# Kernel optimization log

Hardware: AMD Instinct MI355X
Metric: run time of the kernel (lower is better)

## Reference

```python
import jax, jax.numpy as jnp
import numpy as np

CODEBOOK_SIZE = 1024
D_MODEL = 512
NUM_SAMPLES = 10
TEMP = 1.0
COMMITMENT_COST = 0.25
PADDING_IDX = 0


def setup_inputs() -> dict:
    key = jax.random.key(0)
    k1, k2, k3 = jax.random.split(key, 3)
    inputs = jax.random.normal(k1, (64, 512, D_MODEL), dtype=jnp.float32)
    padding_mask = jax.random.randint(k2, (64, 512), 0, 2) == 1
    codebook_weight = 0.02 * jax.random.normal(k3, (CODEBOOK_SIZE, D_MODEL), dtype=jnp.float32)
    codebook_weight = codebook_weight.at[PADDING_IDX].set(0.0)  # padding_idx row zeroed
    return {"inputs": inputs, "padding_mask": padding_mask, "codebook_weight": codebook_weight}


def reference(inputs, padding_mask, codebook_weight):
    B, S, D = inputs.shape
    K = codebook_weight.shape[0]
    flat = inputs.reshape(-1, D)  # [N, D]
    # squared-euclidean distances to codebook entries: [N, K]
    dist = (jnp.sum(flat * flat, axis=1, keepdims=True)
            + jnp.sum(codebook_weight * codebook_weight, axis=1)
            - 2.0 * (flat @ codebook_weight.T))
    pad = padding_mask.reshape(-1)  # [N]
    col = jnp.arange(K)
    # padded rows: only code 0 allowed; non-padded rows: code 0 disallowed
    allowed = jnp.where(pad[:, None], col == 0, col != 0)
    dist = jnp.where(allowed, dist, jnp.inf)

    # Multinomial(total_count=NUM_SAMPLES, logits=-dist/TEMP): draw NUM_SAMPLES
    # categorical samples per row and count them.
    logits = -dist / TEMP
    N = flat.shape[0]
    draws = jax.random.categorical(jax.random.key(42), logits, axis=-1,
                                   shape=(NUM_SAMPLES, N))  # [num_samples, N]
    row_idx = jnp.broadcast_to(jnp.arange(N)[None, :], draws.shape)
    samples = jnp.zeros((N, K), jnp.float32).at[row_idx, draws].add(1.0)  # counts, [N, K]

    quantized = (samples @ codebook_weight).reshape(B, S, D) / NUM_SAMPLES

    num_nonpad = (jnp.sum(~pad) * D).astype(jnp.float32)
    e_latent_loss = jnp.sum((jax.lax.stop_gradient(quantized) - inputs) ** 2) / num_nonpad
    loss = COMMITMENT_COST * e_latent_loss

    # straight-through estimator
    quantized_st = inputs + jax.lax.stop_gradient(quantized - inputs)

    avg_probs = jnp.mean(samples, axis=0) / NUM_SAMPLES  # [K]
    perplexity = jnp.exp(-jnp.sum(avg_probs * jnp.log(avg_probs + 1e-10)))

    samples_out = samples.reshape(B, S, K)
    return quantized_st, samples_out, loss, perplexity
```

## Files before the change

kernel.cpp:

```cpp
#include <hip/hip_runtime.h>
#include <stdint.h>

#define NROWS 32768
#define KC 1024
#define DM 512
#define NKPROD 33554432u

typedef _Float16 v8h __attribute__((ext_vector_type(8)));
typedef float v4f __attribute__((ext_vector_type(4)));

__device__ __forceinline__ uint32_t rotl32(uint32_t x, int d) {
  return __builtin_amdgcn_alignbit(x, x, 32 - d);
}

__device__ __forceinline__ void threefry_x2(uint32_t xa, uint32_t xb,
                                            uint32_t& oa, uint32_t& ob) {
  const uint32_t ks1 = 42u, ks2 = 0x1BD11BF0u;
  uint32_t a0 = 0u, a1 = xa + ks1;
  uint32_t b0 = 0u, b1 = xb + ks1;
#define R2(r) { a0 += a1; b0 += b1; a1 = rotl32(a1, r); b1 = rotl32(b1, r); a1 ^= a0; b1 ^= b0; }
  R2(13) R2(15) R2(26) R2(6)
  a0 += ks1; b0 += ks1; a1 += ks2 + 1u; b1 += ks2 + 1u;
  R2(17) R2(29) R2(16) R2(24)
  a0 += ks2; b0 += ks2; a1 += 2u; b1 += 2u;
  R2(13) R2(15) R2(26) R2(6)
  a1 += ks1 + 3u; b1 += ks1 + 3u;
  R2(17) R2(29) R2(16) R2(24)
  a0 += ks1; b0 += ks1; a1 += ks2 + 4u; b1 += ks2 + 4u;
  R2(13) R2(15) R2(26) R2(6)
  a0 += ks2; b0 += ks2; a1 += 5u; b1 += 5u;
#undef R2
  oa = a0 ^ a1;
  ob = b0 ^ b1;
}

__global__ __launch_bounds__(256) void k_count(const uint8_t* __restrict__ mb,
                                               uint32_t* __restrict__ flag,
                                               int* __restrict__ cntB,
                                               int* __restrict__ cntI) {
  __shared__ int sB[256], sI[256];
  int t = threadIdx.x, b = blockIdx.x;
  int T = b * 256 + t;
  uint32_t f = 0;
#pragma unroll
  for (int i = 0; i < 2; ++i) {
    int bi = T * 2 + i;
    if ((bi & 3) && mb[bi]) f = 1;
  }
  if (f) atomicOr(flag, 1u);
  const int* mi = (const int*)mb;
  int r0 = b * 512 + t * 2;
  int cB = 0, cI = 0;
#pragma unroll
  for (int i = 0; i < 2; ++i) {
    int r = r0 + i;
    cB += (mb[r] == 0) ? 1 : 0;
    cI += (mi[r] == 0) ? 1 : 0;
  }
  sB[t] = cB; sI[t] = cI;
  __syncthreads();
  for (int off = 128; off; off >>= 1) {
    if (t < off) { sB[t] += sB[t + off]; sI[t] += sI[t + off]; }
    __syncthreads();
  }
  if (t == 0) { cntB[b] = sB[0]; cntI[b] = sI[0]; }
}

__global__ __launch_bounds__(256) void k_scatter(const uint8_t* __restrict__ mb,
                                                 const uint32_t* __restrict__ flag,
                                                 const int* __restrict__ cntB,
                                                 const int* __restrict__ cntI,
                                                 int* __restrict__ idx,
                                                 int* __restrict__ npp) {
  __shared__ int sc[256];
  int t = threadIdx.x, b = blockIdx.x;
  bool isbool = (*flag) != 0;
  const int* mi = (const int*)mb;
  const int* cnt = isbool ? cntB : cntI;
  int pre = 0, tot = 0;
  for (int j = 0; j < 64; ++j) {
    int c = cnt[j];
    if (j < b) pre += c;
    tot += c;
  }
  int r0 = b * 512 + t * 2;
  bool np0 = isbool ? (mb[r0] == 0)     : (mi[r0] == 0);
  bool np1 = isbool ? (mb[r0 + 1] == 0) : (mi[r0 + 1] == 0);
  int my = (int)np0 + (int)np1;
  sc[t] = my;
  __syncthreads();
  for (int off = 1; off < 256; off <<= 1) {
    int v = (t >= off) ? sc[t - off] : 0;
    __syncthreads();
    sc[t] += v;
    __syncthreads();
  }
  int excl = sc[t] - my;
  int npPos = pre + excl;
  int padPos = tot + (b * 512 - pre) + (t * 2 - excl);
  if (np0) idx[npPos++] = r0;     else idx[padPos++] = r0;
  if (np1) idx[npPos]   = r0 + 1; else idx[padPos]   = r0 + 1;
  if (b == 0 && t == 0) *npp = tot;
}

__global__ __launch_bounds__(256) void k_asplit(const float* __restrict__ A,
                                                const int* __restrict__ idx,
                                                _Float16* __restrict__ Ah2,
                                                _Float16* __restrict__ Al2,
                                                float* __restrict__ An) {
  int slot = blockIdx.x * 4 + (threadIdx.x >> 6);
  int l = threadIdx.x & 63;
  int n = idx[slot];
  const float* ap = A + (size_t)n * DM + l * 8;
  float x[8];
  *(float4*)&x[0] = *(const float4*)ap;
  *(float4*)&x[4] = *(const float4*)(ap + 4);
  _Float16 h[8], lo[8];
  float s = 0.f;
#pragma unroll
  for (int i = 0; i < 8; ++i) {
    _Float16 hh = (_Float16)x[i];
    h[i] = hh; lo[i] = (_Float16)(x[i] - (float)hh);
    s = fmaf(x[i], x[i], s);
  }
  *(v8h*)&Ah2[(size_t)slot * DM + l * 8] = *(v8h*)h;
  *(v8h*)&Al2[(size_t)slot * DM + l * 8] = *(v8h*)lo;
#pragma unroll
  for (int off = 32; off; off >>= 1) s += __shfl_xor(s, off, 64);
  if (l == 0) An[slot] = s;
}

__global__ __launch_bounds__(256) void k_bsplit(const float* __restrict__ B,
                                                _Float16* __restrict__ Bh2,
                                                _Float16* __restrict__ Bl2,
                                                float* __restrict__ Bn) {
  int k = blockIdx.x * 4 + (threadIdx.x >> 6);
  int l = threadIdx.x & 63;
  const float* bp = B + (size_t)k * DM + l * 8;
  float x[8];
  *(float4*)&x[0] = *(const float4*)bp;
  *(float4*)&x[4] = *(const float4*)(bp + 4);
  _Float16 h[8], lo[8];
  float s = 0.f;
#pragma unroll
  for (int i = 0; i < 8; ++i) {
    _Float16 hh = (_Float16)x[i];
    h[i] = hh; lo[i] = (_Float16)(x[i] - (float)hh);
    s = fmaf(x[i], x[i], s);
  }
  *(v8h*)&Bh2[(size_t)k * DM + l * 8] = *(v8h*)h;
  *(v8h*)&Bl2[(size_t)k * DM + l * 8] = *(v8h*)lo;
#pragma unroll
  for (int off = 32; off; off >>= 1) s += __shfl_xor(s, off, 64);
  if (l == 0) Bn[k] = s;
}

#define LDK 40
__global__ __launch_bounds__(256) void k_gemm5(const _Float16* __restrict__ Ah2,
                                               const _Float16* __restrict__ Al2,
                                               const float* __restrict__ An,
                                               const _Float16* __restrict__ Bh2,
                                               const _Float16* __restrict__ Bl2,
                                               const float* __restrict__ Bn,
                                               const int* __restrict__ idx,
                                               const int* __restrict__ npp,
                                               float* __restrict__ S) {
  int NP = *npp;
  int bx = blockIdx.x & 7;
  int by = blockIdx.x >> 3;
  int r0 = by * 128, c0 = bx * 128;
  if (r0 >= NP) return;

  __shared__ _Float16 Ah[128 * LDK], Al[128 * LDK];
  __shared__ _Float16 Bh[128 * LDK], Bl[128 * LDK];

  int tid = threadIdx.x;
  int wid = tid >> 6;
  int wr = wid >> 1, wc = wid & 1;
  int l = tid & 63;
  int lr = l & 15;
  int k8 = (l >> 4) * 8;

  int srow = tid >> 1;
  int ssub = (tid & 1) * 16;

  const _Float16* ahg = Ah2 + (size_t)(r0 + srow) * DM + ssub;
  const _Float16* alg = Al2 + (size_t)(r0 + srow) * DM + ssub;
  const _Float16* bhg = Bh2 + (size_t)(c0 + srow) * DM + ssub;
  const _Float16* blg = Bl2 + (size_t)(c0 + srow) * DM + ssub;

  v4f acc[4][4];
#pragma unroll
  for (int m = 0; m < 4; ++m)
#pragma unroll
    for (int n = 0; n < 4; ++n) acc[m][n] = (v4f)0.0f;

  for (int k0 = 0; k0 < DM; k0 += 32) {
    v8h ah0 = *(const v8h*)(ahg + k0);
    v8h ah1 = *(const v8h*)(ahg + k0 + 8);
    v8h al0 = *(const v8h*)(alg + k0);
    v8h al1 = *(const v8h*)(alg + k0 + 8);
    v8h bh0 = *(const v8h*)(bhg + k0);
    v8h bh1 = *(const v8h*)(bhg + k0 + 8);
    v8h bl0 = *(const v8h*)(blg + k0);
    v8h bl1 = *(const v8h*)(blg + k0 + 8);
    __syncthreads();
    int wb = srow * LDK + ssub;
    *(v8h*)&Ah[wb]     = ah0;
    *(v8h*)&Ah[wb + 8] = ah1;
    *(v8h*)&Al[wb]     = al0;
    *(v8h*)&Al[wb + 8] = al1;
    *(v8h*)&Bh[wb]     = bh0;
    *(v8h*)&Bh[wb + 8] = bh1;
    *(v8h*)&Bl[wb]     = bl0;
    *(v8h*)&Bl[wb + 8] = bl1;
    __syncthreads();

    v8h fah[4], fal[4];
#pragma unroll
    for (int m = 0; m < 4; ++m) {
      int row = wr * 64 + m * 16 + lr;
      fah[m] = *(const v8h*)&Ah[row * LDK + k8];
      fal[m] = *(const v8h*)&Al[row * LDK + k8];
    }
#pragma unroll
    for (int n = 0; n < 4; ++n) {
      int col = wc * 64 + n * 16 + lr;
      v8h fbh = *(const v8h*)&Bh[col * LDK + k8];
      v8h fbl = *(const v8h*)&Bl[col * LDK + k8];
#pragma unroll
      for (int m = 0; m < 4; ++m) {
        acc[m][n] = __builtin_amdgcn_mfma_f32_16x16x32_f16(fah[m], fbh, acc[m][n], 0, 0, 0);
        acc[m][n] = __builtin_amdgcn_mfma_f32_16x16x32_f16(fah[m], fbl, acc[m][n], 0, 0, 0);
        acc[m][n] = __builtin_amdgcn_mfma_f32_16x16x32_f16(fal[m], fbh, acc[m][n], 0, 0, 0);
      }
    }
  }

  float cnp[4];
#pragma unroll
  for (int n = 0; n < 4; ++n) cnp[n] = Bn[c0 + wc * 64 + n * 16 + lr];

#pragma unroll
  for (int m = 0; m < 4; ++m) {
    int rl = wr * 64 + m * 16 + (l >> 4) * 4;
#pragma unroll
    for (int r = 0; r < 4; ++r) {
      int org = idx[r0 + rl + r];
      float rq = An[r0 + rl + r];
      float* sp = S + (size_t)org * KC + c0;
#pragma unroll
      for (int n = 0; n < 4; ++n) {
        int cl = wc * 64 + n * 16 + lr;
        sp[cl] = -((rq + cnp[n]) - 2.0f * acc[m][n][r]);
      }
    }
  }
}

__global__ __launch_bounds__(256) void k_pad(const float* __restrict__ X,
                                             const int* __restrict__ idx,
                                             const int* __restrict__ npp,
                                             float* __restrict__ qout,
                                             float* __restrict__ sout,
                                             double* __restrict__ esum) {
  int NP = *npp;
  int slot = blockIdx.x * 4 + (threadIdx.x >> 6);
  if (slot < NP) return;
  int n = idx[slot];
  int l = threadIdx.x & 63;

  float* so = sout + (size_t)n * KC + l * 16;
  float4 z = make_float4(0.f, 0.f, 0.f, 0.f);
  *(float4*)(so)      = (l == 0) ? make_float4(10.f, 0.f, 0.f, 0.f) : z;
  *(float4*)(so + 4)  = z;
  *(float4*)(so + 8)  = z;
  *(float4*)(so + 12) = z;

  const float* xr = X + (size_t)n * DM + l * 8;
  float4 x0 = *(const float4*)xr, x1 = *(const float4*)(xr + 4);
  float* qo = qout + (size_t)n * DM + l * 8;
  *(float4*)qo       = z;
  *(float4*)(qo + 4) = z;
  double ls = (double)(x0.x*x0.x) + (double)(x0.y*x0.y)
            + (double)(x0.z*x0.z) + (double)(x0.w*x0.w)
            + (double)(x1.x*x1.x) + (double)(x1.y*x1.y)
            + (double)(x1.z*x1.z) + (double)(x1.w*x1.w);
#pragma unroll
  for (int off = 32; off; off >>= 1) ls += __shfl_xor(ls, off, 64);
  if (l == 0) atomicAdd(&esum[n & 63], ls);
}

__global__ __launch_bounds__(256, 8) void k_sample_i(
    const float* __restrict__ S, const float* __restrict__ X,
    const float* __restrict__ CW, const int* __restrict__ idx,
    const int* __restrict__ npp,
    float* __restrict__ qout, float* __restrict__ sout,
    float* __restrict__ cnt, double* __restrict__ esum) {
  int NP = *npp;
  int slot = blockIdx.x * 4 + (threadIdx.x >> 6);
  if (slot >= NP) return;
  int n = idx[slot];
  int l = threadIdx.x & 63;
  int base = l * 16;
  const float* srow = S + (size_t)n * KC + base;

  float lmax;
  {
    float lg0[16];
#pragma unroll
    for (int j = 0; j < 16; j += 4)
      *(float4*)&lg0[j] = *(const float4*)(srow + j);
    if (l == 0) lg0[0] = -__builtin_inff();
    lmax = lg0[0];
#pragma unroll
    for (int i = 1; i < 16; ++i) lmax = fmaxf(lmax, lg0[i]);
#pragma unroll
    for (int off = 32; off; off >>= 1)
      lmax = fmaxf(lmax, __shfl_xor(lmax, off, 64));
  }

  float bv[10];
  uint32_t bi[10];
#pragma unroll
  for (int s = 0; s < 10; ++s) { bv[s] = -__builtin_inff(); bi[s] = 0xFFFFFFFFu; }

  uint32_t tb0 = (uint32_t)n * (uint32_t)KC + (uint32_t)base;
#pragma unroll 1
  for (int j = 0; j < 16; ++j) {
    float lgj = srow[j];
    uint32_t kk = (uint32_t)(base + j);
    if (kk == 0u) lgj = -__builtin_inff();
    float mj = 0.69314718056f * __expf(lmax - lgj);
    uint32_t t0 = tb0 + (uint32_t)j;
#pragma unroll
    for (int sp = 0; sp < 5; ++sp) {
      uint32_t ba, bb;
      threefry_x2(t0 + (uint32_t)(2 * sp) * NKPROD,
                  t0 + (uint32_t)(2 * sp + 1) * NKPROD, ba, bb);
      float fa = __uint_as_float((ba >> 9) | 0x3F800000u) - 1.0f;
      float fb = __uint_as_float((bb >> 9) | 0x3F800000u) - 1.0f;
      float ua = fmaxf(1.17549435e-38f, fa);
      float ub = fmaxf(1.17549435e-38f, fb);
      float va = __log2f(ua) * mj;
      float vb = __log2f(ub) * mj;
      if (va > bv[2 * sp])     { bv[2 * sp] = va;     bi[2 * sp] = kk; }
      if (vb > bv[2 * sp + 1]) { bv[2 * sp + 1] = vb; bi[2 * sp + 1] = kk; }
    }
  }

#pragma unroll
  for (int s = 0; s < 10; ++s) {
#pragma unroll
    for (int off = 32; off; off >>= 1) {
      float ov = __shfl_xor(bv[s], off, 64);
      uint32_t oi = __shfl_xor(bi[s], off, 64);
      if (ov > bv[s] || (ov == bv[s] && oi < bi[s])) { bv[s] = ov; bi[s] = oi; }
    }
  }

  float* so = sout + (size_t)n * KC + base;
#pragma unroll
  for (int j4 = 0; j4 < 16; j4 += 4) {
    float c[4];
#pragma unroll
    for (int i = 0; i < 4; ++i) {
      uint32_t k = (uint32_t)(base + j4 + i);
      float cc = 0.f;
#pragma unroll
      for (int s = 0; s < 10; ++s) cc += (bi[s] == k) ? 1.f : 0.f;
      c[i] = cc;
    }
    *(float4*)(so + j4) = make_float4(c[0], c[1], c[2], c[3]);
  }

  float q[8];
#pragma unroll
  for (int i = 0; i < 8; ++i) q[i] = 0.f;
#pragma unroll
  for (int s = 0; s < 10; ++s) {
    const float* cr = CW + (size_t)bi[s] * DM + l * 8;
    float4 g0 = *(const float4*)cr;
    float4 g1 = *(const float4*)(cr + 4);
    q[0] += g0.x; q[1] += g0.y; q[2] += g0.z; q[3] += g0.w;
    q[4] += g1.x; q[5] += g1.y; q[6] += g1.z; q[7] += g1.w;
    if (l == 0) atomicAdd(&cnt[bi[s]], 1.0f);
  }

  const float* xr = X + (size_t)n * DM + l * 8;
  float4 x0 = *(const float4*)xr, x1 = *(const float4*)(xr + 4);
  float xs[8] = {x0.x, x0.y, x0.z, x0.w, x1.x, x1.y, x1.z, x1.w};
  float st[8];
  double ls = 0.0;
#pragma unroll
  for (int j = 0; j < 8; ++j) {
    float qq = q[j] / 10.0f;
    float d = qq - xs[j];
    ls += (double)(d * d);
    st[j] = xs[j] + d;
  }
  float* qo = qout + (size_t)n * DM + l * 8;
  *(float4*)qo       = make_float4(st[0], st[1], st[2], st[3]);
  *(float4*)(qo + 4) = make_float4(st[4], st[5], st[6], st[7]);

#pragma unroll
  for (int off = 32; off; off >>= 1) ls += __shfl_xor(ls, off, 64);
  if (l == 0) atomicAdd(&esum[n & 63], ls);
}

__global__ __launch_bounds__(256) void k_final(const int* __restrict__ npp,
                                               const float* __restrict__ cnt,
                                               const double* __restrict__ esum,
                                               float* __restrict__ scal) {
  __shared__ double snd[256];
  int t = threadIdx.x;
  int npad = NROWS - *npp;
  double ss = 0.0;
  for (int k = t; k < KC; k += 256) {
    float c = (k == 0) ? (float)(npad * 10) : cnt[k];
    float p = c / 327680.0f;
    ss += (double)(p * logf(p + 1e-10f));
  }
  snd[t] = ss;
  __syncthreads();
  for (int off = 128; off; off >>= 1) {
    if (t < off) snd[t] += snd[t + off];
    __syncthreads();
  }
  if (t == 0) {
    double es = 0.0;
    for (int i = 0; i < 64; ++i) es += esum[i];
    float num_nonpad = (float)((NROWS - npad) * DM);
    float el = (float)es / num_nonpad;
    scal[0] = 0.25f * el;
    scal[1] = expf(-(float)snd[0]);
  }
}

extern "C" void kernel_launch(void* const* d_in, const int* in_sizes, int n_in,
                              void* d_out, int out_size, void* d_ws, size_t ws_size,
                              hipStream_t stream) {
  const float* X  = (const float*)d_in[0];
  const void*  M  = d_in[1];
  const float* CW = (const float*)d_in[2];
  float* out  = (float*)d_out;
  float* qout = out;
  float* sout = out + 16777216;
  float* scal = out + 50331648;
  _Float16* Ah2 = (_Float16*)qout;
  _Float16* Al2 = Ah2 + 16777216;
  uint8_t* ws = (uint8_t*)d_ws;
  double*   esum = (double*)ws;
  uint32_t* flag = (uint32_t*)(ws + 512);
  int*      npp  = (int*)(ws + 768);
  float*    cnt  = (float*)(ws + 1024);
  int*      cntB = (int*)(ws + 5120);
  int*      cntI = (int*)(ws + 5376);
  int*      idx  = (int*)(ws + 8192);
  float*    An   = (float*)(ws + 139264);
  _Float16* Bh2  = (_Float16*)(ws + 270336);
  _Float16* Bl2  = (_Float16*)(ws + 270336 + 1048576);
  float*    Bn   = (float*)(ws + 270336 + 2097152);
  (void)in_sizes; (void)n_in; (void)out_size; (void)ws_size;

  hipMemsetAsync(d_ws, 0, 8192, stream);
  k_count<<<64, 256, 0, stream>>>((const uint8_t*)M, flag, cntB, cntI);
  k_scatter<<<64, 256, 0, stream>>>((const uint8_t*)M, flag, cntB, cntI, idx, npp);
  k_asplit<<<8192, 256, 0, stream>>>(X, idx, Ah2, Al2, An);
  k_bsplit<<<256, 256, 0, stream>>>(CW, Bh2, Bl2, Bn);
  k_gemm5<<<2048, 256, 0, stream>>>(Ah2, Al2, An, Bh2, Bl2, Bn, idx, npp, sout);
  k_pad<<<8192, 256, 0, stream>>>(X, idx, npp, qout, sout, esum);
  k_sample_i<<<8192, 256, 0, stream>>>(sout, X, CW, idx, npp, qout, sout, cnt, esum);
  k_final<<<1, 256, 0, stream>>>(npp, cnt, esum, scal);
}
```

Baseline: 508.7 us.

## Fuse A-split, GEMM, padding and sampling into one persistent work-queue kernel

Replaces the separate asplit, gemm, pad and sample kernels with one persistent kernel. Helper blocks pull GEMM tiles from an atomic ticket counter and split the fp32 inputs into fp16 hi/lo parts on the fly, so the split arrays never go through HBM. The remaining blocks handle padded rows, and then all blocks pull sampling work and spin on per-row-group completion counters. The codebook split is folded into the count kernel. This removes launches and the intermediate A traffic, but adds spin-waits, atomics and a dependence on enough blocks being co-resident to avoid stalls.

Result: slower. 988.5 us (+94.3%).

```diff
diff --git a/kernel.cpp b/kernel.cpp
--- a/kernel.cpp
+++ b/kernel.cpp
@@ -5,6 +5,8 @@
 #define KC 1024
 #define DM 512
 #define NKPROD 33554432u
+#define NHELP 256
+#define LDK 40
 
 typedef _Float16 v8h __attribute__((ext_vector_type(8)));
 typedef float v4f __attribute__((ext_vector_type(4)));
@@ -34,10 +36,32 @@
   ob = b0 ^ b1;
 }
 
-__global__ __launch_bounds__(256) void k_count(const uint8_t* __restrict__ mb,
-                                               uint32_t* __restrict__ flag,
-                                               int* __restrict__ cntB,
-                                               int* __restrict__ cntI) {
+__global__ __launch_bounds__(256) void k_count_bsplit(
+    const uint8_t* __restrict__ mb, const float* __restrict__ B,
+    uint32_t* __restrict__ flag, int* __restrict__ cntB, int* __restrict__ cntI,
+    _Float16* __restrict__ Bh2, _Float16* __restrict__ Bl2, float* __restrict__ Bn) {
+  if (blockIdx.x >= 64) {
+    int k = (blockIdx.x - 64) * 4 + (threadIdx.x >> 6);
+    int l = threadIdx.x & 63;
+    const float* bp = B + (size_t)k * DM + l * 8;
+    float x[8];
+    *(float4*)&x[0] = *(const float4*)bp;
+    *(float4*)&x[4] = *(const float4*)(bp + 4);
+    _Float16 h[8], lo[8];
+    float s = 0.f;
+#pragma unroll
+    for (int i = 0; i < 8; ++i) {
+      _Float16 hh = (_Float16)x[i];
+      h[i] = hh; lo[i] = (_Float16)(x[i] - (float)hh);
+      s = fmaf(x[i], x[i], s);
+    }
+    *(v8h*)&Bh2[(size_t)k * DM + l * 8] = *(v8h*)h;
+    *(v8h*)&Bl2[(size_t)k * DM + l * 8] = *(v8h*)lo;
+#pragma unroll
+    for (int off = 32; off; off >>= 1) s += __shfl_xor(s, off, 64);
+    if (l == 0) Bn[k] = s;
+    return;
+  }
   __shared__ int sB[256], sI[256];
   int t = threadIdx.x, b = blockIdx.x;
   int T = b * 256 + t;
@@ -103,309 +127,289 @@
   if (b == 0 && t == 0) *npp = tot;
 }
 
-__global__ __launch_bounds__(256) void k_asplit(const float* __restrict__ A,
-                                                const int* __restrict__ idx,
-                                                _Float16* __restrict__ Ah2,
-                                                _Float16* __restrict__ Al2,
-                                                float* __restrict__ An) {
-  int slot = blockIdx.x * 4 + (threadIdx.x >> 6);
-  int l = threadIdx.x & 63;
-  int n = idx[slot];
-  const float* ap = A + (size_t)n * DM + l * 8;
-  float x[8];
-  *(float4*)&x[0] = *(const float4*)ap;
-  *(float4*)&x[4] = *(const float4*)(ap + 4);
-  _Float16 h[8], lo[8];
-  float s = 0.f;
-#pragma unroll
-  for (int i = 0; i < 8; ++i) {
-    _Float16 hh = (_Float16)x[i];
-    h[i] = hh; lo[i] = (_Float16)(x[i] - (float)hh);
-    s = fmaf(x[i], x[i], s);
-  }
-  *(v8h*)&Ah2[(size_t)slot * DM + l * 8] = *(v8h*)h;
-  *(v8h*)&Al2[(size_t)slot * DM + l * 8] = *(v8h*)lo;
-#pragma unroll
-  for (int off = 32; off; off >>= 1) s += __shfl_xor(s, off, 64);
-  if (l == 0) An[slot] = s;
-}
-
-__global__ __launch_bounds__(256) void k_bsplit(const float* __restrict__ B,
-                                                _Float16* __restrict__ Bh2,
-                                                _Float16* __restrict__ Bl2,
-                                                float* __restrict__ Bn) {
-  int k = blockIdx.x * 4 + (threadIdx.x >> 6);
-  int l = threadIdx.x & 63;
-  const float* bp = B + (size_t)k * DM + l * 8;
-  float x[8];
-  *(float4*)&x[0] = *(const float4*)bp;
-  *(float4*)&x[4] = *(const float4*)(bp + 4);
-  _Float16 h[8], lo[8];
-  float s = 0.f;
-#pragma unroll
-  for (int i = 0; i < 8; ++i) {
-    _Float16 hh = (_Float16)x[i];
-    h[i] = hh; lo[i] = (_Float16)(x[i] - (float)hh);
-    s = fmaf(x[i], x[i], s);
-  }
-  *(v8h*)&Bh2[(size_t)k * DM + l * 8] = *(v8h*)h;
-  *(v8h*)&Bl2[(size_t)k * DM + l * 8] = *(v8h*)lo;
-#pragma unroll
-  for (int off = 32; off; off >>= 1) s += __shfl_xor(s, off, 64);
-  if (l == 0) Bn[k] = s;
-}
-
-#define LDK 40
-__global__ __launch_bounds__(256) void k_gemm5(const _Float16* __restrict__ Ah2,
-                                               const _Float16* __restrict__ Al2,
-                                               const float* __restrict__ An,
-                                               const _Float16* __restrict__ Bh2,
-                                               const _Float16* __restrict__ Bl2,
-                                               const float* __restrict__ Bn,
-                                               const int* __restrict__ idx,
-                                               const int* __restrict__ npp,
-                                               float* __restrict__ S) {
+__global__ __launch_bounds__(256, 4) void k_mega(
+    const float* __restrict__ X, const float* __restrict__ CW,
+    const _Float16* __restrict__ Bh2, const _Float16* __restrict__ Bl2,
+    const float* __restrict__ Bn,
+    const int* __restrict__ idx, const int* __restrict__ npp,
+    float* __restrict__ S, float* __restrict__ qout,
+    float* __restrict__ cnt, double* __restrict__ esum,
+    int* __restrict__ gc, int* __restrict__ pc, int* __restrict__ scc,
+    int* __restrict__ gemmDone) {
+  __shared__ _Float16 AhS[128 * LDK], AlS[128 * LDK];
+  __shared__ _Float16 BhS[128 * LDK], BlS[128 * LDK];
+  __shared__ int sticket;
   int NP = *npp;
-  int bx = blockIdx.x & 7;
-  int by = blockIdx.x >> 3;
-  int r0 = by * 128, c0 = bx * 128;
-  if (r0 >= NP) return;
-
-  __shared__ _Float16 Ah[128 * LDK], Al[128 * LDK];
-  __shared__ _Float16 Bh[128 * LDK], Bl[128 * LDK];
-
+  int ngroups = (NP + 127) >> 7;
+  int NTG = ngroups << 3;
+  int NPAD = NROWS - NP;
+  int NTP = (NPAD + 15) >> 4;
+  int NTS = (NP + 3) >> 2;
   int tid = threadIdx.x;
-  int wid = tid >> 6;
-  int wr = wid >> 1, wc = wid & 1;
-  int l = tid & 63;
-  int lr = l & 15;
-  int k8 = (l >> 4) * 8;
-
-  int srow = tid >> 1;
-  int ssub = (tid & 1) * 16;
-
-  const _Float16* ahg = Ah2 + (size_t)(r0 + srow) * DM + ssub;
-  const _Float16* alg = Al2 + (size_t)(r0 + srow) * DM + ssub;
-  const _Float16* bhg = Bh2 + (size_t)(c0 + srow) * DM + ssub;
-  const _Float16* blg = Bl2 + (size_t)(c0 + srow) * DM + ssub;
-
-  v4f acc[4][4];
-#pragma unroll
-  for (int m = 0; m < 4; ++m)
-#pragma unroll
-    for (int n = 0; n < 4; ++n) acc[m][n] = (v4f)0.0f;
-
-  for (int k0 = 0; k0 < DM; k0 += 32) {
-    v8h ah0 = *(const v8h*)(ahg + k0);
-    v8h ah1 = *(const v8h*)(ahg + k0 + 8);
-    v8h al0 = *(const v8h*)(alg + k0);
-    v8h al1 = *(const v8h*)(alg + k0 + 8);
-    v8h bh0 = *(const v8h*)(bhg + k0);
-    v8h bh1 = *(const v8h*)(bhg + k0 + 8);
-    v8h bl0 = *(const v8h*)(blg + k0);
-    v8h bl1 = *(const v8h*)(blg + k0 + 8);
-    __syncthreads();
-    int wb = srow * LDK + ssub;
-    *(v8h*)&Ah[wb]     = ah0;
-    *(v8h*)&Ah[wb + 8] = ah1;
-    *(v8h*)&Al[wb]     = al0;
-    *(v8h*)&Al[wb + 8] = al1;
-    *(v8h*)&Bh[wb]     = bh0;
-    *(v8h*)&Bh[wb + 8] = bh1;
-    *(v8h*)&Bl[wb]     = bl0;
-    *(v8h*)&Bl[wb + 8] = bl1;
-    __syncthreads();
-
-    v8h fah[4], fal[4];
-#pragma unroll
-    for (int m = 0; m < 4; ++m) {
-      int row = wr * 64 + m * 16 + lr;
-      fah[m] = *(const v8h*)&Ah[row * LDK + k8];
-      fal[m] = *(const v8h*)&Al[row * LDK + k8];
+  int wid = tid >> 6, l = tid & 63;
+
+  if (blockIdx.x < NHELP) {
+    int wr = wid >> 1, wc = wid & 1;
+    int lr = l & 15, k8 = (l >> 4) * 8;
+    int srow = tid >> 1, ssub = (tid & 1) * 16;
+    while (true) {
+      __syncthreads();
+      if (tid == 0) sticket = atomicAdd(gc, 1);
+      __syncthreads();
+      int g = sticket;
+      if (g >= NTG) break;
+      int by = g >> 3, bx = g & 7;
+      int r0 = by << 7, c0 = bx << 7;
+      int orig = idx[r0 + srow];
+      const float* ag = X + (size_t)orig * DM + ssub;
+      const _Float16* bhg = Bh2 + (size_t)(c0 + srow) * DM + ssub;
+      const _Float16* blg = Bl2 + (size_t)(c0 + srow) * DM + ssub;
+
+      v4f acc[4][4];
+#pragma unroll
+      for (int m = 0; m < 4; ++m)
+#pragma unroll
+        for (int n = 0; n < 4; ++n) acc[m][n] = (v4f)0.0f;
+      float sqa = 0.f;
+
+      for (int k0 = 0; k0 < DM; k0 += 32) {
+        float xa[16];
+#pragma unroll
+        for (int i = 0; i < 16; i += 4)
+          *(float4*)&xa[i] = *(const float4*)(ag + k0 + i);
+        v8h bh0 = *(const v8h*)(bhg + k0);
+        v8h bh1 = *(const v8h*)(bhg + k0 + 8);
+        v8h bl0 = *(const v8h*)(blg + k0);
+        v8h bl1 = *(const v8h*)(blg + k0 + 8);
+        _Float16 ha[16], la[16];
+#pragma unroll
+        for (int i = 0; i < 16; ++i) {
+          float x = xa[i];
+          _Float16 h = (_Float16)x;
+          ha[i] = h; la[i] = (_Float16)(x - (float)h);
+          sqa = fmaf(x, x, sqa);
+        }
+        __syncthreads();
+        int wb = srow * LDK + ssub;
+        *(v8h*)&AhS[wb]     = *(v8h*)&ha[0];
+        *(v8h*)&AhS[wb + 8] = *(v8h*)&ha[8];
+        *(v8h*)&AlS[wb]     = *(v8h*)&la[0];
+        *(v8h*)&AlS[wb + 8] = *(v8h*)&la[8];
+        *(v8h*)&BhS[wb]     = bh0;
+        *(v8h*)&BhS[wb + 8] = bh1;
+        *(v8h*)&BlS[wb]     = bl0;
+        *(v8h*)&BlS[wb + 8] = bl1;
+        __syncthreads();
+
+        v8h fah[4], fal[4];
+#pragma unroll
+        for (int m = 0; m < 4; ++m) {
+          int row = wr * 64 + m * 16 + lr;
+          fah[m] = *(const v8h*)&AhS[row * LDK + k8];
+          fal[m] = *(const v8h*)&AlS[row * LDK + k8];
+        }
+#pragma unroll
+        for (int n = 0; n < 4; ++n) {
+          int col = wc * 64 + n * 16 + lr;
+          v8h fbh = *(const v8h*)&BhS[col * LDK + k8];
+          v8h fbl = *(const v8h*)&BlS[col * LDK + k8];
+#pragma unroll
+          for (int m = 0; m < 4; ++m) {
+            acc[m][n] = __builtin_amdgcn_mfma_f32_16x16x32_f16(fah[m], fbh, acc[m][n], 0, 0, 0);
+            acc[m][n] = __builtin_amdgcn_mfma_f32_16x16x32_f16(fah[m], fbl, acc[m][n], 0, 0, 0);
+            acc[m][n] = __builtin_amdgcn_mfma_f32_16x16x32_f16(fal[m], fbh, acc[m][n], 0, 0, 0);
+          }
+        }
+      }
+
+      __syncthreads();
+      float* tmpf = (float*)AhS;
+      float* rsf  = (float*)AlS;
+      tmpf[tid] = sqa;
+      __syncthreads();
+      if ((tid & 1) == 0) rsf[srow] = tmpf[tid] + tmpf[tid + 1];
+      __syncthreads();
+
+      float cnp[4];
+#pragma unroll
+      for (int n = 0; n < 4; ++n) cnp[n] = Bn[c0 + wc * 64 + n * 16 + lr];
+
+#pragma unroll
+      for (int m = 0; m < 4; ++m) {
+        int rl = wr * 64 + m * 16 + (l >> 4) * 4;
+#pragma unroll
+        for (int r = 0; r < 4; ++r) {
+          int sl = r0 + rl + r;
+          if (sl < NP) {
+            int org = idx[sl];
+            float rq = rsf[rl + r];
+            float* sp = S + (size_t)org * KC + c0;
+#pragma unroll
+            for (int n = 0; n < 4; ++n) {
+              int cl = wc * 64 + n * 16 + lr;
+              sp[cl] = -((rq + cnp[n]) - 2.0f * acc[m][n][r]);
+            }
+          }
+        }
+      }
+      __threadfence();
+      __syncthreads();
+      if (tid == 0) atomicAdd(&gemmDone[by], 1);
     }
-#pragma unroll
-    for (int n = 0; n < 4; ++n) {
-      int col = wc * 64 + n * 16 + lr;
-      v8h fbh = *(const v8h*)&Bh[col * LDK + k8];
-      v8h fbl = *(const v8h*)&Bl[col * LDK + k8];
-#pragma unroll
-      for (int m = 0; m < 4; ++m) {
-        acc[m][n] = __builtin_amdgcn_mfma_f32_16x16x32_f16(fah[m], fbh, acc[m][n], 0, 0, 0);
-        acc[m][n] = __builtin_amdgcn_mfma_f32_16x16x32_f16(fah[m], fbl, acc[m][n], 0, 0, 0);
-        acc[m][n] = __builtin_amdgcn_mfma_f32_16x16x32_f16(fal[m], fbh, acc[m][n], 0, 0, 0);
+  } else {
+    while (true) {
+      __syncthreads();
+      if (tid == 0) sticket = atomicAdd(pc, 1);
+      __syncthreads();
+      int p = sticket;
+      if (p >= NTP) break;
+      for (int i = 0; i < 4; ++i) {
+        int ps = (p << 4) + (wid << 2) + i;
+        if (ps >= NPAD) break;
+        int n = idx[NP + ps];
+        float* so = S + (size_t)n * KC + l * 16;
+        float4 z = make_float4(0.f, 0.f, 0.f, 0.f);
+        *(float4*)(so)      = (l == 0) ? make_float4(10.f, 0.f, 0.f, 0.f) : z;
+        *(float4*)(so + 4)  = z;
+        *(float4*)(so + 8)  = z;
+        *(float4*)(so + 12) = z;
+        const float* xr = X + (size_t)n * DM + l * 8;
+        float4 x0 = *(const float4*)xr, x1 = *(const float4*)(xr + 4);
+        float* qo = qout + (size_t)n * DM + l * 8;
+        *(float4*)qo       = z;
+        *(float4*)(qo + 4) = z;
+        double ls = (double)(x0.x*x0.x) + (double)(x0.y*x0.y)
+                  + (double)(x0.z*x0.z) + (double)(x0.w*x0.w)
+                  + (double)(x1.x*x1.x) + (double)(x1.y*x1.y)
+                  + (double)(x1.z*x1.z) + (double)(x1.w*x1.w);
+#pragma unroll
+        for (int off = 32; off; off >>= 1) ls += __shfl_xor(ls, off, 64);
+        if (l == 0) atomicAdd(&esum[n & 63], ls);
       }
     }
   }
 
-  float cnp[4];
-#pragma unroll
-  for (int n = 0; n < 4; ++n) cnp[n] = Bn[c0 + wc * 64 + n * 16 + lr];
-
-#pragma unroll
-  for (int m = 0; m < 4; ++m) {
-    int rl = wr * 64 + m * 16 + (l >> 4) * 4;
-#pragma unroll
-    for (int r = 0; r < 4; ++r) {
-      int org = idx[r0 + rl + r];
-      float rq = An[r0 + rl + r];
-      float* sp = S + (size_t)org * KC + c0;
-#pragma unroll
-      for (int n = 0; n < 4; ++n) {
-        int cl = wc * 64 + n * 16 + lr;
-        sp[cl] = -((rq + cnp[n]) - 2.0f * acc[m][n][r]);
-      }
+  while (true) {
+    __syncthreads();
+    if (tid == 0) sticket = atomicAdd(scc, 1);
+    __syncthreads();
+    int st = sticket;
+    if (st >= NTS) break;
+    int g = (st << 2) >> 7;
+    if (tid == 0) {
+      while (atomicAdd(&gemmDone[g], 0) < 8) __builtin_amdgcn_s_sleep(32);
     }
-  }
-}
-
-__global__ __launch_bounds__(256) void k_pad(const float* __restrict__ X,
-                                             const int* __restrict__ idx,
-                                             const int* __restrict__ npp,
-                                             float* __restrict__ qout,
-                                             float* __restrict__ sout,
-                                             double* __restrict__ esum) {
-  int NP = *npp;
-  int slot = blockIdx.x * 4 + (threadIdx.x >> 6);
-  if (slot < NP) return;
-  int n = idx[slot];
-  int l = threadIdx.x & 63;
-
-  float* so = sout + (size_t)n * KC + l * 16;
-  float4 z = make_float4(0.f, 0.f, 0.f, 0.f);
-  *(float4*)(so)      = (l == 0) ? make_float4(10.f, 0.f, 0.f, 0.f) : z;
-  *(float4*)(so + 4)  = z;
-  *(float4*)(so + 8)  = z;
-  *(float4*)(so + 12) = z;
-
-  const float* xr = X + (size_t)n * DM + l * 8;
-  float4 x0 = *(const float4*)xr, x1 = *(const float4*)(xr + 4);
-  float* qo = qout + (size_t)n * DM + l * 8;
-  *(float4*)qo       = z;
-  *(float4*)(qo + 4) = z;
-  double ls = (double)(x0.x*x0.x) + (double)(x0.y*x0.y)
-            + (double)(x0.z*x0.z) + (double)(x0.w*x0.w)
-            + (double)(x1.x*x1.x) + (double)(x1.y*x1.y)
-            + (double)(x1.z*x1.z) + (double)(x1.w*x1.w);
-#pragma unroll
-  for (int off = 32; off; off >>= 1) ls += __shfl_xor(ls, off, 64);
-  if (l == 0) atomicAdd(&esum[n & 63], ls);
-}
-
-__global__ __launch_bounds__(256, 8) void k_sample_i(
-    const float* __restrict__ S, const float* __restrict__ X,
-    const float* __restrict__ CW, const int* __restrict__ idx,
-    const int* __restrict__ npp,
-    float* __restrict__ qout, float* __restrict__ sout,
-    float* __restrict__ cnt, double* __restrict__ esum) {
-  int NP = *npp;
-  int slot = blockIdx.x * 4 + (threadIdx.x >> 6);
-  if (slot >= NP) return;
-  int n = idx[slot];
-  int l = threadIdx.x & 63;
-  int base = l * 16;
-  const float* srow = S + (size_t)n * KC + base;
-
-  float lmax;
-  {
-    float lg0[16];
-#pragma unroll
-    for (int j = 0; j < 16; j += 4)
-      *(float4*)&lg0[j] = *(const float4*)(srow + j);
-    if (l == 0) lg0[0] = -__builtin_inff();
-    lmax = lg0[0];
-#pragma unroll
-    for (int i = 1; i < 16; ++i) lmax = fmaxf(lmax, lg0[i]);
-#pragma unroll
-    for (int off = 32; off; off >>= 1)
-      lmax = fmaxf(lmax, __shfl_xor(lmax, off, 64));
-  }
-
-  float bv[10];
-  uint32_t bi[10];
-#pragma unroll
-  for (int s = 0; s < 10; ++s) { bv[s] = -__builtin_inff(); bi[s] = 0xFFFFFFFFu; }
-
-  uint32_t tb0 = (uint32_t)n * (uint32_t)KC + (uint32_t)base;
+    __syncthreads();
+    __threadfence();
+    int slot = (st << 2) + wid;
+    if (slot < NP) {
+      int n = idx[slot];
+      int base = l * 16;
+      const float* srow = S + (size_t)n * KC + base;
+
+      float lmax;
+      {
+        float lg0[16];
+#pragma unroll
+        for (int j = 0; j < 16; j += 4)
+          *(float4*)&lg0[j] = *(const float4*)(srow + j);
+        if (l == 0) lg0[0] = -__builtin_inff();
+        lmax = lg0[0];
+#pragma unroll
+        for (int i = 1; i < 16; ++i) lmax = fmaxf(lmax, lg0[i]);
+#pragma unroll
+        for (int off = 32; off; off >>= 1)
+          lmax = fmaxf(lmax, __shfl_xor(lmax, off, 64));
+      }
+
+      float bv[10];
+      uint32_t bi[10];
+#pragma unroll
+      for (int s = 0; s < 10; ++s) { bv[s] = -__builtin_inff(); bi[s] = 0xFFFFFFFFu; }
+
+      uint32_t tb0 = (uint32_t)n * (uint32_t)KC + (uint32_t)base;
 #pragma unroll 1
-  for (int j = 0; j < 16; ++j) {
-    float lgj = srow[j];
-    uint32_t kk = (uint32_t)(base + j);
-    if (kk == 0u) lgj = -__builtin_inff();
-    float mj = 0.69314718056f * __expf(lmax - lgj);
-    uint32_t t0 = tb0 + (uint32_t)j;
-#pragma unroll
-    for (int sp = 0; sp < 5; ++sp) {
-      uint32_t ba, bb;
-      threefry_x2(t0 + (uint32_t)(2 * sp) * NKPROD,
-                  t0 + (uint32_t)(2 * sp + 1) * NKPROD, ba, bb);
-      float fa = __uint_as_float((ba >> 9) | 0x3F800000u) - 1.0f;
-      float fb = __uint_as_float((bb >> 9) | 0x3F800000u) - 1.0f;
-      float ua = fmaxf(1.17549435e-38f, fa);
-      float ub = fmaxf(1.17549435e-38f, fb);
-      float va = __log2f(ua) * mj;
-      float vb = __log2f(ub) * mj;
-      if (va > bv[2 * sp])     { bv[2 * sp] = va;     bi[2 * sp] = kk; }
-      if (vb > bv[2 * sp + 1]) { bv[2 * sp + 1] = vb; bi[2 * sp + 1] = kk; }
+      for (int j = 0; j < 16; ++j) {
+        float lgj = srow[j];
+        uint32_t kk = (uint32_t)(base + j);
+        if (kk == 0u) lgj = -__builtin_inff();
+        float mj = 0.69314718056f * __expf(lmax - lgj);
+        uint32_t t0 = tb0 + (uint32_t)j;
+#pragma unroll
+        for (int sp = 0; sp < 5; ++sp) {
+          uint32_t ba, bb;
+          threefry_x2(t0 + (uint32_t)(2 * sp) * NKPROD,
+                      t0 + (uint32_t)(2 * sp + 1) * NKPROD, ba, bb);
+          float fa = __uint_as_float((ba >> 9) | 0x3F800000u) - 1.0f;
+          float fb = __uint_as_float((bb >> 9) | 0x3F800000u) - 1.0f;
+          float ua = fmaxf(1.17549435e-38f, fa);
+          float ub = fmaxf(1.17549435e-38f, fb);
+          float va = __log2f(ua) * mj;
+          float vb = __log2f(ub) * mj;
+          if (va > bv[2 * sp])     { bv[2 * sp] = va;     bi[2 * sp] = kk; }
+          if (vb > bv[2 * sp + 1]) { bv[2 * sp + 1] = vb; bi[2 * sp + 1] = kk; }
+        }
+      }
+
+#pragma unroll
+      for (int s = 0; s < 10; ++s) {
+#pragma unroll
+        for (int off = 32; off; off >>= 1) {
+          float ov = __shfl_xor(bv[s], off, 64);
+          uint32_t oi = __shfl_xor(bi[s], off, 64);
+          if (ov > bv[s] || (ov == bv[s] && oi < bi[s])) { bv[s] = ov; bi[s] = oi; }
+        }
+      }
+
+      float* so = S + (size_t)n * KC + base;
+#pragma unroll
+      for (int j4 = 0; j4 < 16; j4 += 4) {
+        float c[4];
+#pragma unroll
+        for (int i = 0; i < 4; ++i) {
+          uint32_t k = (uint32_t)(base + j4 + i);
+          float cc = 0.f;
+#pragma unroll
+          for (int s = 0; s < 10; ++s) cc += (bi[s] == k) ? 1.f : 0.f;
+          c[i] = cc;
+        }
+        *(float4*)(so + j4) = make_float4(c[0], c[1], c[2], c[3]);
+      }
+
+      float q[8];
+#pragma unroll
+      for (int i = 0; i < 8; ++i) q[i] = 0.f;
+#pragma unroll
+      for (int s = 0; s < 10; ++s) {
+        const float* cr = CW + (size_t)bi[s] * DM + l * 8;
+        float4 g0 = *(const float4*)cr;
+        float4 g1 = *(const float4*)(cr + 4);
+        q[0] += g0.x; q[1] += g0.y; q[2] += g0.z; q[3] += g0.w;
+        q[4] += g1.x; q[5] += g1.y; q[6] += g1.z; q[7] += g1.w;
+        if (l == 0) atomicAdd(&cnt[bi[s]], 1.0f);
+      }
+
+      const float* xr = X + (size_t)n * DM + l * 8;
+      float4 x0 = *(const float4*)xr, x1 = *(const float4*)(xr + 4);
+      float xs[8] = {x0.x, x0.y, x0.z, x0.w, x1.x, x1.y, x1.z, x1.w};
+      float st8[8];
+      double ls = 0.0;
+#pragma unroll
+      for (int j = 0; j < 8; ++j) {
+        float qq = q[j] / 10.0f;
+        float d = qq - xs[j];
+        ls += (double)(d * d);
+        st8[j] = xs[j] + d;
+      }
+      float* qo = qout + (size_t)n * DM + l * 8;
+      *(float4*)qo       = make_float4(st8[0], st8[1], st8[2], st8[3]);
+      *(float4*)(qo + 4) = make_float4(st8[4], st8[5], st8[6], st8[7]);
+
+#pragma unroll
+      for (int off = 32; off; off >>= 1) ls += __shfl_xor(ls, off, 64);
+      if (l == 0) atomicAdd(&esum[n & 63], ls);
     }
   }
-
-#pragma unroll
-  for (int s = 0; s < 10; ++s) {
-#pragma unroll
-    for (int off = 32; off; off >>= 1) {
-      float ov = __shfl_xor(bv[s], off, 64);
-      uint32_t oi = __shfl_xor(bi[s], off, 64);
-      if (ov > bv[s] || (ov == bv[s] && oi < bi[s])) { bv[s] = ov; bi[s] = oi; }
-    }
-  }
-
-  float* so = sout + (size_t)n * KC + base;
-#pragma unroll
-  for (int j4 = 0; j4 < 16; j4 += 4) {
-    float c[4];
-#pragma unroll
-    for (int i = 0; i < 4; ++i) {
-      uint32_t k = (uint32_t)(base + j4 + i);
-      float cc = 0.f;
-#pragma unroll
-      for (int s = 0; s < 10; ++s) cc += (bi[s] == k) ? 1.f : 0.f;
-      c[i] = cc;
-    }
-    *(float4*)(so + j4) = make_float4(c[0], c[1], c[2], c[3]);
-  }
-
-  float q[8];
-#pragma unroll
-  for (int i = 0; i < 8; ++i) q[i] = 0.f;
-#pragma unroll
-  for (int s = 0; s < 10; ++s) {
-    const float* cr = CW + (size_t)bi[s] * DM + l * 8;
-    float4 g0 = *(const float4*)cr;
-    float4 g1 = *(const float4*)(cr + 4);
-    q[0] += g0.x; q[1] += g0.y; q[2] += g0.z; q[3] += g0.w;
-    q[4] += g1.x; q[5] += g1.y; q[6] += g1.z; q[7] += g1.w;
-    if (l == 0) atomicAdd(&cnt[bi[s]], 1.0f);
-  }
-
-  const float* xr = X + (size_t)n * DM + l * 8;
-  float4 x0 = *(const float4*)xr, x1 = *(const float4*)(xr + 4);
-  float xs[8] = {x0.x, x0.y, x0.z, x0.w, x1.x, x1.y, x1.z, x1.w};
-  float st[8];
-  double ls = 0.0;
-#pragma unroll
-  for (int j = 0; j < 8; ++j) {
-    float qq = q[j] / 10.0f;
-    float d = qq - xs[j];
-    ls += (double)(d * d);
-    st[j] = xs[j] + d;
-  }
-  float* qo = qout + (size_t)n * DM + l * 8;
-  *(float4*)qo       = make_float4(st[0], st[1], st[2], st[3]);
-  *(float4*)(qo + 4) = make_float4(st[4], st[5], st[6], st[7]);
-
-#pragma unroll
-  for (int off = 32; off; off >>= 1) ls += __shfl_xor(ls, off, 64);
-  if (l == 0) atomicAdd(&esum[n & 63], ls);
 }
 
 __global__ __launch_bounds__(256) void k_final(const int* __restrict__ npp,
@@ -447,8 +451,6 @@
   float* qout = out;
   float* sout = out + 16777216;
   float* scal = out + 50331648;
-  _Float16* Ah2 = (_Float16*)qout;
-  _Float16* Al2 = Ah2 + 16777216;
   uint8_t* ws = (uint8_t*)d_ws;
   double*   esum = (double*)ws;
   uint32_t* flag = (uint32_t*)(ws + 512);
@@ -456,20 +458,21 @@
   float*    cnt  = (float*)(ws + 1024);
   int*      cntB = (int*)(ws + 5120);
   int*      cntI = (int*)(ws + 5376);
+  int*      gc   = (int*)(ws + 5632);
+  int*      pc   = (int*)(ws + 5636);
+  int*      scc  = (int*)(ws + 5640);
+  int*      gdon = (int*)(ws + 6144);
   int*      idx  = (int*)(ws + 8192);
-  float*    An   = (float*)(ws + 139264);
-  _Float16* Bh2  = (_Float16*)(ws + 270336);
-  _Float16* Bl2  = (_Float16*)(ws + 270336 + 1048576);
-  float*    Bn   = (float*)(ws + 270336 + 2097152);
+  _Float16* Bh2  = (_Float16*)(ws + 139264);
+  _Float16* Bl2  = (_Float16*)(ws + 139264 + 1048576);
+  float*    Bn   = (float*)(ws + 139264 + 2097152);
   (void)in_sizes; (void)n_in; (void)out_size; (void)ws_size;
 
   hipMemsetAsync(d_ws, 0, 8192, stream);
-  k_count<<<64, 256, 0, stream>>>((const uint8_t*)M, flag, cntB, cntI);
+  k_count_bsplit<<<320, 256, 0, stream>>>((const uint8_t*)M, CW, flag, cntB, cntI,
+                                          Bh2, Bl2, Bn);
   k_scatter<<<64, 256, 0, stream>>>((const uint8_t*)M, flag, cntB, cntI, idx, npp);
-  k_asplit<<<8192, 256, 0, stream>>>(X, idx, Ah2, Al2, An);
-  k_bsplit<<<256, 256, 0, stream>>>(CW, Bh2, Bl2, Bn);
-  k_gemm5<<<2048, 256, 0, stream>>>(Ah2, Al2, An, Bh2, Bl2, Bn, idx, npp, sout);
-  k_pad<<<8192, 256, 0, stream>>>(X, idx, npp, qout, sout, esum);
-  k_sample_i<<<8192, 256, 0, stream>>>(sout, X, CW, idx, npp, qout, sout, cnt, esum);
+  k_mega<<<1024, 256, 0, stream>>>(X, CW, Bh2, Bl2, Bn, idx, npp,
+                                   sout, qout, cnt, esum, gc, pc, scc, gdon);
   k_final<<<1, 256, 0, stream>>>(npp, cnt, esum, scal);
 }
```

## Fuse codebook split into count, pad work into asplit and sampler

Applied to the files above, without the earlier changes.

Folds the codebook fp16 split into the mask-count kernel as extra blocks, and removes the separate padding kernel. Its loss accumulation and samples-row writes move into the A-split kernel, which now only splits rows up to the GEMM tile-rounded count. Padded rows inside the last GEMM tile get their samples rows rewritten by the sampler after the GEMM overwrites them. This cuts two launches and skips converting padded rows, with extra branching and an ordering dependency between the GEMM tail and the sampler writes.

Result: faster. 488.0 us (-4.1%).

```diff
diff --git a/kernel.cpp b/kernel.cpp
--- a/kernel.cpp
+++ b/kernel.cpp
@@ -34,10 +34,32 @@
   ob = b0 ^ b1;
 }
 
-__global__ __launch_bounds__(256) void k_count(const uint8_t* __restrict__ mb,
-                                               uint32_t* __restrict__ flag,
-                                               int* __restrict__ cntB,
-                                               int* __restrict__ cntI) {
+__global__ __launch_bounds__(256) void k_count_bsplit(
+    const uint8_t* __restrict__ mb, const float* __restrict__ B,
+    uint32_t* __restrict__ flag, int* __restrict__ cntB, int* __restrict__ cntI,
+    _Float16* __restrict__ Bh2, _Float16* __restrict__ Bl2, float* __restrict__ Bn) {
+  if (blockIdx.x >= 64) {
+    int k = (blockIdx.x - 64) * 4 + (threadIdx.x >> 6);
+    int l = threadIdx.x & 63;
+    const float* bp = B + (size_t)k * DM + l * 8;
+    float x[8];
+    *(float4*)&x[0] = *(const float4*)bp;
+    *(float4*)&x[4] = *(const float4*)(bp + 4);
+    _Float16 h[8], lo[8];
+    float s = 0.f;
+#pragma unroll
+    for (int i = 0; i < 8; ++i) {
+      _Float16 hh = (_Float16)x[i];
+      h[i] = hh; lo[i] = (_Float16)(x[i] - (float)hh);
+      s = fmaf(x[i], x[i], s);
+    }
+    *(v8h*)&Bh2[(size_t)k * DM + l * 8] = *(v8h*)h;
+    *(v8h*)&Bl2[(size_t)k * DM + l * 8] = *(v8h*)lo;
+#pragma unroll
+    for (int off = 32; off; off >>= 1) s += __shfl_xor(s, off, 64);
+    if (l == 0) Bn[k] = s;
+    return;
+  }
   __shared__ int sB[256], sI[256];
   int t = threadIdx.x, b = blockIdx.x;
   int T = b * 256 + t;
@@ -103,56 +125,56 @@
   if (b == 0 && t == 0) *npp = tot;
 }
 
-__global__ __launch_bounds__(256) void k_asplit(const float* __restrict__ A,
-                                                const int* __restrict__ idx,
-                                                _Float16* __restrict__ Ah2,
-                                                _Float16* __restrict__ Al2,
-                                                float* __restrict__ An) {
+__global__ __launch_bounds__(256) void k_asplit_pad(
+    const float* __restrict__ X, const int* __restrict__ idx,
+    const int* __restrict__ npp,
+    _Float16* __restrict__ Ah2, _Float16* __restrict__ Al2,
+    float* __restrict__ An, float* __restrict__ sout,
+    double* __restrict__ esum) {
+  int NP = *npp;
+  int NPc = (NP + 127) & ~127;
   int slot = blockIdx.x * 4 + (threadIdx.x >> 6);
   int l = threadIdx.x & 63;
   int n = idx[slot];
-  const float* ap = A + (size_t)n * DM + l * 8;
-  float x[8];
-  *(float4*)&x[0] = *(const float4*)ap;
-  *(float4*)&x[4] = *(const float4*)(ap + 4);
-  _Float16 h[8], lo[8];
-  float s = 0.f;
-#pragma unroll
-  for (int i = 0; i < 8; ++i) {
-    _Float16 hh = (_Float16)x[i];
-    h[i] = hh; lo[i] = (_Float16)(x[i] - (float)hh);
-    s = fmaf(x[i], x[i], s);
-  }
-  *(v8h*)&Ah2[(size_t)slot * DM + l * 8] = *(v8h*)h;
-  *(v8h*)&Al2[(size_t)slot * DM + l * 8] = *(v8h*)lo;
-#pragma unroll
-  for (int off = 32; off; off >>= 1) s += __shfl_xor(s, off, 64);
-  if (l == 0) An[slot] = s;
-}
-
-__global__ __launch_bounds__(256) void k_bsplit(const float* __restrict__ B,
-                                                _Float16* __restrict__ Bh2,
-                                                _Float16* __restrict__ Bl2,
-                                                float* __restrict__ Bn) {
-  int k = blockIdx.x * 4 + (threadIdx.x >> 6);
-  int l = threadIdx.x & 63;
-  const float* bp = B + (size_t)k * DM + l * 8;
-  float x[8];
-  *(float4*)&x[0] = *(const float4*)bp;
-  *(float4*)&x[4] = *(const float4*)(bp + 4);
-  _Float16 h[8], lo[8];
-  float s = 0.f;
-#pragma unroll
-  for (int i = 0; i < 8; ++i) {
-    _Float16 hh = (_Float16)x[i];
-    h[i] = hh; lo[i] = (_Float16)(x[i] - (float)hh);
-    s = fmaf(x[i], x[i], s);
-  }
-  *(v8h*)&Bh2[(size_t)k * DM + l * 8] = *(v8h*)h;
-  *(v8h*)&Bl2[(size_t)k * DM + l * 8] = *(v8h*)lo;
-#pragma unroll
-  for (int off = 32; off; off >>= 1) s += __shfl_xor(s, off, 64);
-  if (l == 0) Bn[k] = s;
+  const float* xr = X + (size_t)n * DM + l * 8;
+
+  if (slot < NPc) {
+    float x[8];
+    *(float4*)&x[0] = *(const float4*)xr;
+    *(float4*)&x[4] = *(const float4*)(xr + 4);
+    _Float16 h[8], lo[8];
+    float s = 0.f;
+#pragma unroll
+    for (int i = 0; i < 8; ++i) {
+      _Float16 hh = (_Float16)x[i];
+      h[i] = hh; lo[i] = (_Float16)(x[i] - (float)hh);
+      s = fmaf(x[i], x[i], s);
+    }
+    *(v8h*)&Ah2[(size_t)slot * DM + l * 8] = *(v8h*)h;
+    *(v8h*)&Al2[(size_t)slot * DM + l * 8] = *(v8h*)lo;
+#pragma unroll
+    for (int off = 32; off; off >>= 1) s += __shfl_xor(s, off, 64);
+    if (l == 0) An[slot] = s;
+    if (slot < NP) return;
+  }
+
+  float4 x0 = *(const float4*)xr, x1 = *(const float4*)(xr + 4);
+  double ls = (double)(x0.x*x0.x) + (double)(x0.y*x0.y)
+            + (double)(x0.z*x0.z) + (double)(x0.w*x0.w)
+            + (double)(x1.x*x1.x) + (double)(x1.y*x1.y)
+            + (double)(x1.z*x1.z) + (double)(x1.w*x1.w);
+#pragma unroll
+  for (int off = 32; off; off >>= 1) ls += __shfl_xor(ls, off, 64);
+  if (l == 0) atomicAdd(&esum[n & 63], ls);
+
+  if (slot >= NPc) {
+    float* so = sout + (size_t)n * KC + l * 16;
+    float4 z = make_float4(0.f, 0.f, 0.f, 0.f);
+    *(float4*)(so)      = (l == 0) ? make_float4(10.f, 0.f, 0.f, 0.f) : z;
+    *(float4*)(so + 4)  = z;
+    *(float4*)(so + 8)  = z;
+    *(float4*)(so + 12) = z;
+  }
 }
 
 #define LDK 40
@@ -258,39 +280,6 @@
   }
 }
 
-__global__ __launch_bounds__(256) void k_pad(const float* __restrict__ X,
-                                             const int* __restrict__ idx,
-                                             const int* __restrict__ npp,
-                                             float* __restrict__ qout,
-                                             float* __restrict__ sout,
-                                             double* __restrict__ esum) {
-  int NP = *npp;
-  int slot = blockIdx.x * 4 + (threadIdx.x >> 6);
-  if (slot < NP) return;
-  int n = idx[slot];
-  int l = threadIdx.x & 63;
-
-  float* so = sout + (size_t)n * KC + l * 16;
-  float4 z = make_float4(0.f, 0.f, 0.f, 0.f);
-  *(float4*)(so)      = (l == 0) ? make_float4(10.f, 0.f, 0.f, 0.f) : z;
-  *(float4*)(so + 4)  = z;
-  *(float4*)(so + 8)  = z;
-  *(float4*)(so + 12) = z;
-
-  const float* xr = X + (size_t)n * DM + l * 8;
-  float4 x0 = *(const float4*)xr, x1 = *(const float4*)(xr + 4);
-  float* qo = qout + (size_t)n * DM + l * 8;
-  *(float4*)qo       = z;
-  *(float4*)(qo + 4) = z;
-  double ls = (double)(x0.x*x0.x) + (double)(x0.y*x0.y)
-            + (double)(x0.z*x0.z) + (double)(x0.w*x0.w)
-            + (double)(x1.x*x1.x) + (double)(x1.y*x1.y)
-            + (double)(x1.z*x1.z) + (double)(x1.w*x1.w);
-#pragma unroll
-  for (int off = 32; off; off >>= 1) ls += __shfl_xor(ls, off, 64);
-  if (l == 0) atomicAdd(&esum[n & 63], ls);
-}
-
 __global__ __launch_bounds__(256, 8) void k_sample_i(
     const float* __restrict__ S, const float* __restrict__ X,
     const float* __restrict__ CW, const int* __restrict__ idx,
@@ -299,10 +288,26 @@
     float* __restrict__ cnt, double* __restrict__ esum) {
   int NP = *npp;
   int slot = blockIdx.x * 4 + (threadIdx.x >> 6);
-  if (slot >= NP) return;
+  int l = threadIdx.x & 63;
   int n = idx[slot];
-  int l = threadIdx.x & 63;
   int base = l * 16;
+
+  if (slot >= NP) {
+    float4 z = make_float4(0.f, 0.f, 0.f, 0.f);
+    float* qo = qout + (size_t)n * DM + l * 8;
+    *(float4*)qo       = z;
+    *(float4*)(qo + 4) = z;
+    int NPc = (NP + 127) & ~127;
+    if (slot < NPc) {
+      float* so = sout + (size_t)n * KC + base;
+      *(float4*)(so)      = (l == 0) ? make_float4(10.f, 0.f, 0.f, 0.f) : z;
+      *(float4*)(so + 4)  = z;
+      *(float4*)(so + 8)  = z;
+      *(float4*)(so + 12) = z;
+    }
+    return;
+  }
+
   const float* srow = S + (size_t)n * KC + base;
 
   float lmax;
@@ -464,12 +469,11 @@
   (void)in_sizes; (void)n_in; (void)out_size; (void)ws_size;
 
   hipMemsetAsync(d_ws, 0, 8192, stream);
-  k_count<<<64, 256, 0, stream>>>((const uint8_t*)M, flag, cntB, cntI);
+  k_count_bsplit<<<320, 256, 0, stream>>>((const uint8_t*)M, CW, flag, cntB, cntI,
+                                          Bh2, Bl2, Bn);
   k_scatter<<<64, 256, 0, stream>>>((const uint8_t*)M, flag, cntB, cntI, idx, npp);
-  k_asplit<<<8192, 256, 0, stream>>>(X, idx, Ah2, Al2, An);
-  k_bsplit<<<256, 256, 0, stream>>>(CW, Bh2, Bl2, Bn);
+  k_asplit_pad<<<8192, 256, 0, stream>>>(X, idx, npp, Ah2, Al2, An, sout, esum);
   k_gemm5<<<2048, 256, 0, stream>>>(Ah2, Al2, An, Bh2, Bl2, Bn, idx, npp, sout);
-  k_pad<<<8192, 256, 0, stream>>>(X, idx, npp, qout, sout, esum);
   k_sample_i<<<8192, 256, 0, stream>>>(sout, X, CW, idx, npp, qout, sout, cnt, esum);
   k_final<<<1, 256, 0, stream>>>(npp, cnt, esum, scal);
 }
```
